# Performance work log

Hardware: AMD Instinct MI355X
Metric: run time of the kernel (lower is better)

The kernel has to match this reference:

```python
import jax, jax.numpy as jnp
import numpy as np

BN_EPS = 1e-5


def trilinear_sample(feat, grid):
    """F.grid_sample 5D, mode='bilinear', padding_mode='border', align_corners=True.
    feat: (B,C,D,H,W); grid: (B,N,3) in [-1,1], last dim ordered (x,y,z) -> (W,H,D).
    Returns (B,N,C)."""
    B, C, D, H, W = feat.shape
    # align_corners=True unnormalization; border padding == clamp continuous coord
    x = jnp.clip((grid[..., 0] + 1.0) * 0.5 * (W - 1), 0.0, W - 1)
    y = jnp.clip((grid[..., 1] + 1.0) * 0.5 * (H - 1), 0.0, H - 1)
    z = jnp.clip((grid[..., 2] + 1.0) * 0.5 * (D - 1), 0.0, D - 1)
    x0 = jnp.floor(x).astype(jnp.int32); x1 = jnp.minimum(x0 + 1, W - 1)
    y0 = jnp.floor(y).astype(jnp.int32); y1 = jnp.minimum(y0 + 1, H - 1)
    z0 = jnp.floor(z).astype(jnp.int32); z1 = jnp.minimum(z0 + 1, D - 1)
    wx = (x - x0)[:, None, :]  # (B,1,N)
    wy = (y - y0)[:, None, :]
    wz = (z - z0)[:, None, :]
    flat = feat.reshape(B, C, D * H * W)

    def gather(zi, yi, xi):
        idx = (zi * H + yi) * W + xi            # (B,N)
        return jnp.take_along_axis(flat, idx[:, None, :], axis=2)  # (B,C,N)

    c00 = gather(z0, y0, x0) * (1 - wx) + gather(z0, y0, x1) * wx
    c01 = gather(z0, y1, x0) * (1 - wx) + gather(z0, y1, x1) * wx
    c10 = gather(z1, y0, x0) * (1 - wx) + gather(z1, y0, x1) * wx
    c11 = gather(z1, y1, x0) * (1 - wx) + gather(z1, y1, x1) * wx
    c0 = c00 * (1 - wy) + c01 * wy
    c1 = c10 * (1 - wy) + c11 * wy
    out = c0 * (1 - wz) + c1 * wz               # (B,C,N)
    return out.transpose(0, 2, 1)                # (B,N,C)


def batchnorm(x, gamma, beta, mean, var):
    # inference-mode BatchNorm1d over channel (last) dim
    return (x - mean) * jax.lax.rsqrt(var + BN_EPS) * gamma + beta


def setup_inputs() -> dict:
    key = jax.random.key(0)
    ks = jax.random.split(key, 16)
    B, C, D, H, W = 2, 128, 64, 64, 64
    N = 65536
    h1, h2 = 512, 512
    inp = {
        "dense_features": jax.random.normal(ks[0], (B, C, D, H, W), dtype=jnp.float32),
        "query_points": jax.random.uniform(ks[1], (B, N, 3), dtype=jnp.float32),
        "W1": jax.random.normal(ks[2], (C, h1), dtype=jnp.float32) / np.sqrt(C),
        "b1": jax.random.normal(ks[3], (h1,), dtype=jnp.float32) * 0.01,
        "g1": jax.random.uniform(ks[4], (h1,), dtype=jnp.float32, minval=0.5, maxval=1.5),
        "be1": jax.random.normal(ks[5], (h1,), dtype=jnp.float32) * 0.1,
        "m1": jax.random.normal(ks[6], (h1,), dtype=jnp.float32) * 0.1,
        "v1": jax.random.uniform(ks[7], (h1,), dtype=jnp.float32, minval=0.5, maxval=1.5),
        "W2": jax.random.normal(ks[8], (h1, h2), dtype=jnp.float32) / np.sqrt(h1),
        "b2": jax.random.normal(ks[9], (h2,), dtype=jnp.float32) * 0.01,
        "g2": jax.random.uniform(ks[10], (h2,), dtype=jnp.float32, minval=0.5, maxval=1.5),
        "be2": jax.random.normal(ks[11], (h2,), dtype=jnp.float32) * 0.1,
        "m2": jax.random.normal(ks[12], (h2,), dtype=jnp.float32) * 0.1,
        "v2": jax.random.uniform(ks[13], (h2,), dtype=jnp.float32, minval=0.5, maxval=1.5),
        "W3": jax.random.normal(ks[14], (h2, 1), dtype=jnp.float32) / np.sqrt(h2),
        "b3": jax.random.normal(ks[15], (1,), dtype=jnp.float32) * 0.01,
    }
    return inp


def reference(dense_features, query_points, W1, b1, g1, be1, m1, v1,
              W2, b2, g2, be2, m2, v2, W3, b3):
    grid = 2.0 * query_points - 1.0                       # (B,N,3)
    feats = trilinear_sample(dense_features, grid)        # (B,N,128)
    h = jax.nn.relu(batchnorm(jnp.einsum('bnc,ch->bnh', feats, W1) + b1, g1, be1, m1, v1))
    h = jax.nn.relu(batchnorm(jnp.einsum('bnc,ch->bnh', h, W2) + b2, g2, be2, m2, v2))
    out = jnp.einsum('bnc,ch->bnh', h, W3) + b3           # (B,N,1)
    return out
```

## Files before the change

### kernel.cpp

```cpp
#include <hip/hip_runtime.h>
#include <hip/hip_bf16.h>

using bf16x8 = __attribute__((ext_vector_type(8))) short;
using f32x4  = __attribute__((ext_vector_type(4))) float;
using u32x4  = __attribute__((ext_vector_type(4))) unsigned int;
typedef unsigned short u16;
typedef unsigned int u32;

#define NB    2
#define NC    128
#define NPTS  65536
#define MTOT  (NB*NPTS)
#define NTILE (MTOT/64)

static __device__ __forceinline__ u16 f2bf(float f) {
    u32 u = __float_as_uint(f);
    u32 r = (u + 0x7FFFu + ((u >> 16) & 1u)) >> 16;
    return (u16)r;
}
static __device__ __forceinline__ float bflo(u32 d) { return __uint_as_float(d << 16); }
static __device__ __forceinline__ float bfhi(u32 d) { return __uint_as_float(d & 0xFFFF0000u); }

__global__ void prep_kernel(
    const float* __restrict__ W1, const float* __restrict__ W2,
    const float* __restrict__ b1, const float* __restrict__ g1, const float* __restrict__ be1,
    const float* __restrict__ m1, const float* __restrict__ v1,
    const float* __restrict__ b2, const float* __restrict__ g2, const float* __restrict__ be2,
    const float* __restrict__ m2, const float* __restrict__ v2,
    u16* __restrict__ W1p, u16* __restrict__ W2p,
    float* __restrict__ s1, float* __restrict__ t1,
    float* __restrict__ s2, float* __restrict__ t2)
{
    int id = blockIdx.x * 256 + threadIdx.x;
    {
        int l = id & 63, nf = (id >> 6) & 3, kk = (id >> 8) & 15, w = id >> 12;
        int n  = w * 64 + nf * 16 + (l & 15);
        int c0 = kk * 32 + (l >> 4) * 8;
        #pragma unroll
        for (int j = 0; j < 8; ++j)
            W2p[id * 8 + j] = f2bf(W2[(size_t)(c0 + j) * 512 + n]);
    }
    if (id < 8192) {
        int l = id & 63, nf = (id >> 6) & 3, kk = (id >> 8) & 3, w = id >> 10;
        int n  = w * 64 + nf * 16 + (l & 15);
        int c0 = kk * 32 + (l >> 4) * 8;
        #pragma unroll
        for (int j = 0; j < 8; ++j)
            W1p[id * 8 + j] = f2bf(W1[(size_t)(c0 + j) * 512 + n]);
    }
    if (id < 512) {
        float s = g1[id] * rsqrtf(v1[id] + 1e-5f);
        s1[id] = s;
        t1[id] = (b1[id] - m1[id]) * s + be1[id];
        float ss = g2[id] * rsqrtf(v2[id] + 1e-5f);
        s2[id] = ss;
        t2[id] = (b2[id] - m2[id]) * ss + be2[id];
    }
}

__global__ __launch_bounds__(256) void transpose_kernel(const float* __restrict__ feat,
                                                        u16* __restrict__ featT)
{
    __shared__ float tile[128][33];
    int blk = blockIdx.x;
    int b   = blk >> 13;
    int v0  = (blk & 8191) << 5;
    int t   = threadIdx.x;
    int vi  = t & 31;
    int c0  = t >> 5;
    const float* fb = feat + ((size_t)b << 25);
    #pragma unroll
    for (int r = 0; r < 16; ++r) {
        int c = c0 + 8 * r;
        tile[c][vi] = fb[((size_t)c << 18) + v0 + vi];
    }
    __syncthreads();
    u32* outp = (u32*)(featT + (((size_t)b << 18) + v0) * 128);
    #pragma unroll
    for (int r = 0; r < 8; ++r) {
        int w  = t + 256 * r;
        int v  = w >> 6;
        int cp = w & 63;
        float lo = tile[2 * cp][v], hi = tile[2 * cp + 1][v];
        outp[w] = (u32)f2bf(lo) | ((u32)f2bf(hi) << 16);
    }
}

__global__ __launch_bounds__(256) void sampleT_kernel(const u16* __restrict__ featT,
                                                      const float* __restrict__ qp,
                                                      u16* __restrict__ fo)
{
    int tid = blockIdx.x * 256 + threadIdx.x;
    int p   = tid >> 4;
    int li  = tid & 15;
    int b   = p >> 16;

    float qx = qp[p * 3 + 0];
    float qy = qp[p * 3 + 1];
    float qz = qp[p * 3 + 2];
    float x = fminf(fmaxf(qx * 63.0f, 0.0f), 63.0f);
    float y = fminf(fmaxf(qy * 63.0f, 0.0f), 63.0f);
    float z = fminf(fmaxf(qz * 63.0f, 0.0f), 63.0f);
    int x0 = (int)floorf(x), y0 = (int)floorf(y), z0 = (int)floorf(z);
    int x1 = min(x0 + 1, 63), y1 = min(y0 + 1, 63), z1 = min(z0 + 1, 63);
    float wx = x - (float)x0, wy = y - (float)y0, wz = z - (float)z0;

    const u32* fb = (const u32*)featT + ((size_t)b << 24);
    int zy00 = z0 * 4096 + y0 * 64, zy01 = z0 * 4096 + y1 * 64;
    int zy10 = z1 * 4096 + y0 * 64, zy11 = z1 * 4096 + y1 * 64;
    int co = li * 4;
    u32x4 d000 = *(const u32x4*)(fb + (size_t)(zy00 + x0) * 64 + co);
    u32x4 d001 = *(const u32x4*)(fb + (size_t)(zy00 + x1) * 64 + co);
    u32x4 d010 = *(const u32x4*)(fb + (size_t)(zy01 + x0) * 64 + co);
    u32x4 d011 = *(const u32x4*)(fb + (size_t)(zy01 + x1) * 64 + co);
    u32x4 d100 = *(const u32x4*)(fb + (size_t)(zy10 + x0) * 64 + co);
    u32x4 d101 = *(const u32x4*)(fb + (size_t)(zy10 + x1) * 64 + co);
    u32x4 d110 = *(const u32x4*)(fb + (size_t)(zy11 + x0) * 64 + co);
    u32x4 d111 = *(const u32x4*)(fb + (size_t)(zy11 + x1) * 64 + co);

    float omx = 1.0f - wx, omy = 1.0f - wy, omz = 1.0f - wz;
    u32x4 o;
    #pragma unroll
    for (int j = 0; j < 4; ++j) {
        float c00 = bflo(d000[j]) * omx + bflo(d001[j]) * wx;
        float c01 = bflo(d010[j]) * omx + bflo(d011[j]) * wx;
        float c10 = bflo(d100[j]) * omx + bflo(d101[j]) * wx;
        float c11 = bflo(d110[j]) * omx + bflo(d111[j]) * wx;
        float rl  = (c00 * omy + c01 * wy) * omz + (c10 * omy + c11 * wy) * wz;
        float d00 = bfhi(d000[j]) * omx + bfhi(d001[j]) * wx;
        float d01 = bfhi(d010[j]) * omx + bfhi(d011[j]) * wx;
        float d10 = bfhi(d100[j]) * omx + bfhi(d101[j]) * wx;
        float d11 = bfhi(d110[j]) * omx + bfhi(d111[j]) * wx;
        float rh  = (d00 * omy + d01 * wy) * omz + (d10 * omy + d11 * wy) * wz;
        o[j] = (u32)f2bf(rl) | ((u32)f2bf(rh) << 16);
    }
    *(u32x4*)((u32*)fo + (size_t)p * 64 + co) = o;
}

__global__ __launch_bounds__(512, 4) void mlp_kernel(
    const u16* __restrict__ feats, const u16* __restrict__ W1p, const u16* __restrict__ W2p,
    const float* __restrict__ s1, const float* __restrict__ t1,
    const float* __restrict__ s2, const float* __restrict__ t2,
    const float* __restrict__ W3, const float* __restrict__ b3,
    float* __restrict__ out)
{
    __shared__ u16 h1[64 * 512];
    __shared__ float outb[512];

    const int tidx = threadIdx.x;
    const int w    = tidx >> 6;
    const int l    = tidx & 63;
    const int l15  = l & 15;
    const int lq   = l >> 4;
    const int m0   = blockIdx.x * 64;
    const int n0   = w * 64;

    const u16* B1 = W1p + (size_t)(w * 4)  * 4 * 512;
    const u16* B2 = W2p + (size_t)(w * 16) * 4 * 512;

#define LOADA1(dst, kk) { _Pragma("unroll") for (int mf = 0; mf < 4; ++mf) \
    (dst)[mf] = *(const bf16x8*)(feats + (size_t)(m0 + mf * 16 + l15) * 128 + (kk) * 32 + lq * 8); }
#define LOADB1(dst, kk) { _Pragma("unroll") for (int nf = 0; nf < 4; ++nf) \
    (dst)[nf] = *(const bf16x8*)(B1 + ((kk) * 4 + nf) * 512 + l * 8); }
#define LOADB2(dst, kk) { _Pragma("unroll") for (int nf = 0; nf < 4; ++nf) \
    (dst)[nf] = *(const bf16x8*)(B2 + ((kk) * 4 + nf) * 512 + l * 8); }
#define LOADA2(dst, kk) { _Pragma("unroll") for (int mf = 0; mf < 4; ++mf) { \
    int row = mf * 16 + l15; \
    (dst)[mf] = *(const bf16x8*)(h1 + row * 512 + (((kk) * 32 + lq * 8) ^ ((row & 7) << 3))); } }

    f32x4 acc[4][4];
    #pragma unroll
    for (int i = 0; i < 4; ++i)
        #pragma unroll
        for (int j = 0; j < 4; ++j) acc[i][j] = (f32x4){0.f, 0.f, 0.f, 0.f};
    {
        bf16x8 bv[2][4];
        LOADB1(bv[0], 0);
        #pragma unroll
        for (int kk = 0; kk < 4; ++kk) {
            const int cur = kk & 1, nxt = cur ^ 1;
            if (kk < 3) LOADB1(bv[nxt], kk + 1);
            bf16x8 av[4];
            LOADA1(av, kk);
            __builtin_amdgcn_s_setprio(1);
            #pragma unroll
            for (int mf = 0; mf < 4; ++mf)
                #pragma unroll
                for (int nf = 0; nf < 4; ++nf)
                    acc[mf][nf] = __builtin_amdgcn_mfma_f32_16x16x32_bf16(av[mf], bv[cur][nf], acc[mf][nf], 0, 0, 0);
            __builtin_amdgcn_s_setprio(0);
        }
    }

    {
        float s1v[4], t1v[4];
        #pragma unroll
        for (int nf = 0; nf < 4; ++nf) {
            int col = n0 + nf * 16 + l15;
            s1v[nf] = s1[col]; t1v[nf] = t1[col];
        }
        #pragma unroll
        for (int mf = 0; mf < 4; ++mf)
            #pragma unroll
            for (int nf = 0; nf < 4; ++nf) {
                int col = n0 + nf * 16 + l15;
                #pragma unroll
                for (int i = 0; i < 4; ++i) {
                    int row = mf * 16 + lq * 4 + i;
                    float v = fmaxf(acc[mf][nf][i] * s1v[nf] + t1v[nf], 0.0f);
                    h1[row * 512 + (col ^ ((row & 7) << 3))] = f2bf(v);
                }
            }
    }
    __syncthreads();

    f32x4 acc2[4][4];
    #pragma unroll
    for (int i = 0; i < 4; ++i)
        #pragma unroll
        for (int j = 0; j < 4; ++j) acc2[i][j] = (f32x4){0.f, 0.f, 0.f, 0.f};
    {
        bf16x8 pb[2][4];
        LOADB2(pb[0], 0);
        #pragma unroll
        for (int kk = 0; kk < 16; ++kk) {
            const int cur = kk & 1, nxt = cur ^ 1;
            if (kk < 15) LOADB2(pb[nxt], kk + 1);
            bf16x8 a2[4];
            LOADA2(a2, kk);
            __builtin_amdgcn_s_setprio(1);
            #pragma unroll
            for (int mf = 0; mf < 4; ++mf)
                #pragma unroll
                for (int nf = 0; nf < 4; ++nf)
                    acc2[mf][nf] = __builtin_amdgcn_mfma_f32_16x16x32_bf16(a2[mf], pb[cur][nf], acc2[mf][nf], 0, 0, 0);
            __builtin_amdgcn_s_setprio(0);
        }
    }

    float part[16];
    #pragma unroll
    for (int i = 0; i < 16; ++i) part[i] = 0.f;
    {
        float s2v[4], t2v[4], w3v[4];
        #pragma unroll
        for (int nf = 0; nf < 4; ++nf) {
            int col = n0 + nf * 16 + l15;
            s2v[nf] = s2[col]; t2v[nf] = t2[col]; w3v[nf] = W3[col];
        }
        #pragma unroll
        for (int mf = 0; mf < 4; ++mf)
            #pragma unroll
            for (int nf = 0; nf < 4; ++nf)
                #pragma unroll
                for (int i = 0; i < 4; ++i) {
                    float h = fmaxf(acc2[mf][nf][i] * s2v[nf] + t2v[nf], 0.0f);
                    part[mf * 4 + i] += h * w3v[nf];
                }
    }
    #pragma unroll
    for (int off = 1; off < 16; off <<= 1)
        #pragma unroll
        for (int i = 0; i < 16; ++i) part[i] += __shfl_xor(part[i], off, 64);

    if (l15 == 0) {
        #pragma unroll
        for (int mf = 0; mf < 4; ++mf)
            #pragma unroll
            for (int i = 0; i < 4; ++i)
                outb[w * 64 + mf * 16 + lq * 4 + i] = part[mf * 4 + i];
    }
    __syncthreads();
    if (tidx < 64) {
        float r = b3[0];
        #pragma unroll
        for (int ww = 0; ww < 8; ++ww) r += outb[ww * 64 + tidx];
        out[m0 + tidx] = r;
    }
#undef LOADA1
#undef LOADB1
#undef LOADB2
#undef LOADA2
}

__global__ void sample_kernel(const float* __restrict__ feat,
                              const float* __restrict__ qp,
                              u16* __restrict__ fo)
{
    int tid = blockIdx.x * 256 + threadIdx.x;
    int p = tid >> 7;
    int c = tid & 127;
    int b = p >> 16;

    float qx = qp[p * 3 + 0], qy = qp[p * 3 + 1], qz = qp[p * 3 + 2];
    float x = fminf(fmaxf(qx * 63.0f, 0.0f), 63.0f);
    float y = fminf(fmaxf(qy * 63.0f, 0.0f), 63.0f);
    float z = fminf(fmaxf(qz * 63.0f, 0.0f), 63.0f);
    int x0 = (int)floorf(x), y0 = (int)floorf(y), z0 = (int)floorf(z);
    int x1 = min(x0 + 1, 63), y1 = min(y0 + 1, 63), z1 = min(z0 + 1, 63);
    float wx = x - (float)x0, wy = y - (float)y0, wz = z - (float)z0;

    const float* fb = feat + ((size_t)(b * NC + c) << 18);
    int zy00 = z0 * 4096 + y0 * 64, zy01 = z0 * 4096 + y1 * 64;
    int zy10 = z1 * 4096 + y0 * 64, zy11 = z1 * 4096 + y1 * 64;
    float f000 = fb[zy00 + x0], f001 = fb[zy00 + x1];
    float f010 = fb[zy01 + x0], f011 = fb[zy01 + x1];
    float f100 = fb[zy10 + x0], f101 = fb[zy10 + x1];
    float f110 = fb[zy11 + x0], f111 = fb[zy11 + x1];

    float omx = 1.0f - wx;
    float c00 = f000 * omx + f001 * wx;
    float c01 = f010 * omx + f011 * wx;
    float c10 = f100 * omx + f101 * wx;
    float c11 = f110 * omx + f111 * wx;
    float omy = 1.0f - wy;
    float c0 = c00 * omy + c01 * wy;
    float c1 = c10 * omy + c11 * wy;
    float v  = c0 * (1.0f - wz) + c1 * wz;
    fo[(size_t)p * 128 + c] = f2bf(v);
}

extern "C" void kernel_launch(void* const* d_in, const int* in_sizes, int n_in,
                              void* d_out, int out_size, void* d_ws, size_t ws_size,
                              hipStream_t stream)
{
    const float* feat = (const float*)d_in[0];
    const float* qp   = (const float*)d_in[1];
    const float* W1   = (const float*)d_in[2];
    const float* b1   = (const float*)d_in[3];
    const float* g1   = (const float*)d_in[4];
    const float* be1  = (const float*)d_in[5];
    const float* m1   = (const float*)d_in[6];
    const float* v1   = (const float*)d_in[7];
    const float* W2   = (const float*)d_in[8];
    const float* b2   = (const float*)d_in[9];
    const float* g2   = (const float*)d_in[10];
    const float* be2  = (const float*)d_in[11];
    const float* m2   = (const float*)d_in[12];
    const float* v2   = (const float*)d_in[13];
    const float* W3   = (const float*)d_in[14];
    const float* b3   = (const float*)d_in[15];

    char* ws = (char*)d_ws;
    u16*   W1p   = (u16*)(ws);
    u16*   W2p   = (u16*)(ws + 131072);
    float* s1    = (float*)(ws + 655360);
    float* t1    = (float*)(ws + 657408);
    float* s2    = (float*)(ws + 659456);
    float* t2    = (float*)(ws + 661504);
    u16*   feats = (u16*)(ws + 663552);
    u16*   featT = (u16*)(ws + 663552 + 33554432);
    const size_t needed = 663552 + 33554432 + 134217728;

    prep_kernel<<<128, 256, 0, stream>>>(W1, W2, b1, g1, be1, m1, v1,
                                         b2, g2, be2, m2, v2,
                                         W1p, W2p, s1, t1, s2, t2);
    if (ws_size >= needed) {
        transpose_kernel<<<16384, 256, 0, stream>>>(feat, featT);
        sampleT_kernel<<<(MTOT * 16) / 256, 256, 0, stream>>>(featT, qp, feats);
    } else {
        sample_kernel<<<(MTOT * 128) / 256, 256, 0, stream>>>(feat, qp, feats);
    }
    mlp_kernel<<<NTILE, 512, 0, stream>>>(feats, W1p, W2p, s1, t1, s2, t2,
                                          W3, b3, (float*)d_out);
}
```

Before: 212.3 us.

## Fuse trilinear sampling into MLP kernel via LDS tile; vectorize transpose

Result: faster. 177.2 us (-16.5%).

```diff
diff --git a/kernel.cpp b/kernel.cpp
--- a/kernel.cpp
+++ b/kernel.cpp
@@ -66,79 +66,40 @@
     int b   = blk >> 13;
     int v0  = (blk & 8191) << 5;
     int t   = threadIdx.x;
-    int vi  = t & 31;
-    int c0  = t >> 5;
-    const float* fb = feat + ((size_t)b << 25);
-    #pragma unroll
-    for (int r = 0; r < 16; ++r) {
-        int c = c0 + 8 * r;
-        tile[c][vi] = fb[((size_t)c << 18) + v0 + vi];
+    const float* fb = feat + ((size_t)b << 25) + v0;
+    int c_l = t >> 3, f4 = t & 7;
+    #pragma unroll
+    for (int r = 0; r < 4; ++r) {
+        int c = c_l + 32 * r;
+        float4 v = *(const float4*)(fb + ((size_t)c << 18) + f4 * 4);
+        tile[c][f4 * 4 + 0] = v.x;
+        tile[c][f4 * 4 + 1] = v.y;
+        tile[c][f4 * 4 + 2] = v.z;
+        tile[c][f4 * 4 + 3] = v.w;
     }
     __syncthreads();
     u32* outp = (u32*)(featT + (((size_t)b << 18) + v0) * 128);
     #pragma unroll
-    for (int r = 0; r < 8; ++r) {
-        int w  = t + 256 * r;
-        int v  = w >> 6;
-        int cp = w & 63;
-        float lo = tile[2 * cp][v], hi = tile[2 * cp + 1][v];
-        outp[w] = (u32)f2bf(lo) | ((u32)f2bf(hi) << 16);
-    }
-}
-
-__global__ __launch_bounds__(256) void sampleT_kernel(const u16* __restrict__ featT,
-                                                      const float* __restrict__ qp,
-                                                      u16* __restrict__ fo)
-{
-    int tid = blockIdx.x * 256 + threadIdx.x;
-    int p   = tid >> 4;
-    int li  = tid & 15;
-    int b   = p >> 16;
-
-    float qx = qp[p * 3 + 0];
-    float qy = qp[p * 3 + 1];
-    float qz = qp[p * 3 + 2];
-    float x = fminf(fmaxf(qx * 63.0f, 0.0f), 63.0f);
-    float y = fminf(fmaxf(qy * 63.0f, 0.0f), 63.0f);
-    float z = fminf(fmaxf(qz * 63.0f, 0.0f), 63.0f);
-    int x0 = (int)floorf(x), y0 = (int)floorf(y), z0 = (int)floorf(z);
-    int x1 = min(x0 + 1, 63), y1 = min(y0 + 1, 63), z1 = min(z0 + 1, 63);
-    float wx = x - (float)x0, wy = y - (float)y0, wz = z - (float)z0;
-
-    const u32* fb = (const u32*)featT + ((size_t)b << 24);
-    int zy00 = z0 * 4096 + y0 * 64, zy01 = z0 * 4096 + y1 * 64;
-    int zy10 = z1 * 4096 + y0 * 64, zy11 = z1 * 4096 + y1 * 64;
-    int co = li * 4;
-    u32x4 d000 = *(const u32x4*)(fb + (size_t)(zy00 + x0) * 64 + co);
-    u32x4 d001 = *(const u32x4*)(fb + (size_t)(zy00 + x1) * 64 + co);
-    u32x4 d010 = *(const u32x4*)(fb + (size_t)(zy01 + x0) * 64 + co);
-    u32x4 d011 = *(const u32x4*)(fb + (size_t)(zy01 + x1) * 64 + co);
-    u32x4 d100 = *(const u32x4*)(fb + (size_t)(zy10 + x0) * 64 + co);
-    u32x4 d101 = *(const u32x4*)(fb + (size_t)(zy10 + x1) * 64 + co);
-    u32x4 d110 = *(const u32x4*)(fb + (size_t)(zy11 + x0) * 64 + co);
-    u32x4 d111 = *(const u32x4*)(fb + (size_t)(zy11 + x1) * 64 + co);
-
-    float omx = 1.0f - wx, omy = 1.0f - wy, omz = 1.0f - wz;
-    u32x4 o;
-    #pragma unroll
-    for (int j = 0; j < 4; ++j) {
-        float c00 = bflo(d000[j]) * omx + bflo(d001[j]) * wx;
-        float c01 = bflo(d010[j]) * omx + bflo(d011[j]) * wx;
-        float c10 = bflo(d100[j]) * omx + bflo(d101[j]) * wx;
-        float c11 = bflo(d110[j]) * omx + bflo(d111[j]) * wx;
-        float rl  = (c00 * omy + c01 * wy) * omz + (c10 * omy + c11 * wy) * wz;
-        float d00 = bfhi(d000[j]) * omx + bfhi(d001[j]) * wx;
-        float d01 = bfhi(d010[j]) * omx + bfhi(d011[j]) * wx;
-        float d10 = bfhi(d100[j]) * omx + bfhi(d101[j]) * wx;
-        float d11 = bfhi(d110[j]) * omx + bfhi(d111[j]) * wx;
-        float rh  = (d00 * omy + d01 * wy) * omz + (d10 * omy + d11 * wy) * wz;
-        o[j] = (u32)f2bf(rl) | ((u32)f2bf(rh) << 16);
-    }
-    *(u32x4*)((u32*)fo + (size_t)p * 64 + co) = o;
-}
-
-__global__ __launch_bounds__(512, 4) void mlp_kernel(
-    const u16* __restrict__ feats, const u16* __restrict__ W1p, const u16* __restrict__ W2p,
+    for (int r = 0; r < 2; ++r) {
+        int idx = t + 256 * r;
+        int v   = idx >> 4;
+        int c4  = idx & 15;
+        u32x4 o;
+        #pragma unroll
+        for (int k = 0; k < 4; ++k) {
+            float lo = tile[8 * c4 + 2 * k + 0][v];
+            float hi = tile[8 * c4 + 2 * k + 1][v];
+            o[k] = (u32)f2bf(lo) | ((u32)f2bf(hi) << 16);
+        }
+        *(u32x4*)(outp + (size_t)v * 64 + c4 * 4) = o;
+    }
+}
+
+template<bool SAMP>
+__global__ __launch_bounds__(512, 4) void fused_kernel(
+    const u16* __restrict__ featT, const u16* __restrict__ feats,
+    const float* __restrict__ qp,
+    const u16* __restrict__ W1p, const u16* __restrict__ W2p,
     const float* __restrict__ s1, const float* __restrict__ t1,
     const float* __restrict__ s2, const float* __restrict__ t2,
     const float* __restrict__ W3, const float* __restrict__ b3,
@@ -146,6 +107,7 @@
 {
     __shared__ u16 h1[64 * 512];
     __shared__ float outb[512];
+    u16* atile = h1;
 
     const int tidx = threadIdx.x;
     const int w    = tidx >> 6;
@@ -158,15 +120,72 @@
     const u16* B1 = W1p + (size_t)(w * 4)  * 4 * 512;
     const u16* B2 = W2p + (size_t)(w * 16) * 4 * 512;
 
-#define LOADA1(dst, kk) { _Pragma("unroll") for (int mf = 0; mf < 4; ++mf) \
-    (dst)[mf] = *(const bf16x8*)(feats + (size_t)(m0 + mf * 16 + l15) * 128 + (kk) * 32 + lq * 8); }
 #define LOADB1(dst, kk) { _Pragma("unroll") for (int nf = 0; nf < 4; ++nf) \
     (dst)[nf] = *(const bf16x8*)(B1 + ((kk) * 4 + nf) * 512 + l * 8); }
 #define LOADB2(dst, kk) { _Pragma("unroll") for (int nf = 0; nf < 4; ++nf) \
     (dst)[nf] = *(const bf16x8*)(B2 + ((kk) * 4 + nf) * 512 + l * 8); }
+#define LDSA(dst, kk) { _Pragma("unroll") for (int mf = 0; mf < 4; ++mf) { \
+    int row = mf * 16 + l15; \
+    (dst)[mf] = *(const bf16x8*)(atile + row * 128 + ((((kk) * 4 + lq) ^ (row & 7)) << 3)); } }
 #define LOADA2(dst, kk) { _Pragma("unroll") for (int mf = 0; mf < 4; ++mf) { \
     int row = mf * 16 + l15; \
     (dst)[mf] = *(const bf16x8*)(h1 + row * 512 + (((kk) * 32 + lq * 8) ^ ((row & 7) << 3))); } }
+
+    if (SAMP) {
+        const int li = tidx & 15;
+        const int pr = tidx >> 4;
+        const int co = li * 4;
+        #pragma unroll
+        for (int half = 0; half < 2; ++half) {
+            int row = pr + 32 * half;
+            int p   = m0 + row;
+            int b   = p >> 16;
+            float qx = qp[p * 3 + 0], qy = qp[p * 3 + 1], qz = qp[p * 3 + 2];
+            float x = fminf(fmaxf(qx * 63.0f, 0.0f), 63.0f);
+            float y = fminf(fmaxf(qy * 63.0f, 0.0f), 63.0f);
+            float z = fminf(fmaxf(qz * 63.0f, 0.0f), 63.0f);
+            int x0 = (int)floorf(x), y0 = (int)floorf(y), z0 = (int)floorf(z);
+            int x1 = min(x0 + 1, 63), y1 = min(y0 + 1, 63), z1 = min(z0 + 1, 63);
+            float wx = x - (float)x0, wy = y - (float)y0, wz = z - (float)z0;
+            const u32* fb = (const u32*)featT + ((size_t)b << 24);
+            int zy00 = z0 * 4096 + y0 * 64, zy01 = z0 * 4096 + y1 * 64;
+            int zy10 = z1 * 4096 + y0 * 64, zy11 = z1 * 4096 + y1 * 64;
+            u32x4 d000 = *(const u32x4*)(fb + (size_t)(zy00 + x0) * 64 + co);
+            u32x4 d001 = *(const u32x4*)(fb + (size_t)(zy00 + x1) * 64 + co);
+            u32x4 d010 = *(const u32x4*)(fb + (size_t)(zy01 + x0) * 64 + co);
+            u32x4 d011 = *(const u32x4*)(fb + (size_t)(zy01 + x1) * 64 + co);
+            u32x4 d100 = *(const u32x4*)(fb + (size_t)(zy10 + x0) * 64 + co);
+            u32x4 d101 = *(const u32x4*)(fb + (size_t)(zy10 + x1) * 64 + co);
+            u32x4 d110 = *(const u32x4*)(fb + (size_t)(zy11 + x0) * 64 + co);
+            u32x4 d111 = *(const u32x4*)(fb + (size_t)(zy11 + x1) * 64 + co);
+            float omx = 1.0f - wx, omy = 1.0f - wy, omz = 1.0f - wz;
+            u32x4 o;
+            #pragma unroll
+            for (int j = 0; j < 4; ++j) {
+                float c00 = bflo(d000[j]) * omx + bflo(d001[j]) * wx;
+                float c01 = bflo(d010[j]) * omx + bflo(d011[j]) * wx;
+                float c10 = bflo(d100[j]) * omx + bflo(d101[j]) * wx;
+                float c11 = bflo(d110[j]) * omx + bflo(d111[j]) * wx;
+                float rl  = (c00 * omy + c01 * wy) * omz + (c10 * omy + c11 * wy) * wz;
+                float e00 = bfhi(d000[j]) * omx + bfhi(d001[j]) * wx;
+                float e01 = bfhi(d010[j]) * omx + bfhi(d011[j]) * wx;
+                float e10 = bfhi(d100[j]) * omx + bfhi(d101[j]) * wx;
+                float e11 = bfhi(d110[j]) * omx + bfhi(d111[j]) * wx;
+                float rh  = (e00 * omy + e01 * wy) * omz + (e10 * omy + e11 * wy) * wz;
+                o[j] = (u32)f2bf(rl) | ((u32)f2bf(rh) << 16);
+            }
+            *(u32x4*)(atile + row * 128 + ((li ^ (row & 7)) << 3)) = o;
+        }
+    } else {
+        #pragma unroll
+        for (int r2 = 0; r2 < 2; ++r2) {
+            int idx = tidx + 512 * r2;
+            int row = idx >> 4, ch = idx & 15;
+            u32x4 v = *(const u32x4*)(feats + (size_t)(m0 + row) * 128 + ch * 8);
+            *(u32x4*)(atile + row * 128 + ((ch ^ (row & 7)) << 3)) = v;
+        }
+    }
+    __syncthreads();
 
     f32x4 acc[4][4];
     #pragma unroll
@@ -181,7 +200,7 @@
             const int cur = kk & 1, nxt = cur ^ 1;
             if (kk < 3) LOADB1(bv[nxt], kk + 1);
             bf16x8 av[4];
-            LOADA1(av, kk);
+            LDSA(av, kk);
             __builtin_amdgcn_s_setprio(1);
             #pragma unroll
             for (int mf = 0; mf < 4; ++mf)
@@ -191,6 +210,10 @@
             __builtin_amdgcn_s_setprio(0);
         }
     }
+
+    bf16x8 pb[2][4];
+    LOADB2(pb[0], 0);
+    __syncthreads();
 
     {
         float s1v[4], t1v[4];
@@ -220,8 +243,6 @@
         #pragma unroll
         for (int j = 0; j < 4; ++j) acc2[i][j] = (f32x4){0.f, 0.f, 0.f, 0.f};
     {
-        bf16x8 pb[2][4];
-        LOADB2(pb[0], 0);
         #pragma unroll
         for (int kk = 0; kk < 16; ++kk) {
             const int cur = kk & 1, nxt = cur ^ 1;
@@ -277,9 +298,9 @@
         for (int ww = 0; ww < 8; ++ww) r += outb[ww * 64 + tidx];
         out[m0 + tidx] = r;
     }
-#undef LOADA1
 #undef LOADB1
 #undef LOADB2
+#undef LDSA
 #undef LOADA2
 }
 
@@ -357,10 +378,11 @@
                                          W1p, W2p, s1, t1, s2, t2);
     if (ws_size >= needed) {
         transpose_kernel<<<16384, 256, 0, stream>>>(feat, featT);
-        sampleT_kernel<<<(MTOT * 16) / 256, 256, 0, stream>>>(featT, qp, feats);
+        fused_kernel<true><<<NTILE, 512, 0, stream>>>(featT, feats, qp, W1p, W2p,
+                                                      s1, t1, s2, t2, W3, b3, (float*)d_out);
     } else {
         sample_kernel<<<(MTOT * 128) / 256, 256, 0, stream>>>(feat, qp, feats);
-    }
-    mlp_kernel<<<NTILE, 512, 0, stream>>>(feats, W1p, W2p, s1, t1, s2, t2,
-                                          W3, b3, (float*)d_out);
-}
+        fused_kernel<false><<<NTILE, 512, 0, stream>>>(featT, feats, qp, W1p, W2p,
+                                                       s1, t1, s2, t2, W3, b3, (float*)d_out);
+    }
+}
```
